# Kernel optimization log

Measured on AMD Instinct MI355X. Metric: run time of the kernel, lower is better.

The kernel has to match this reference:

```python
import jax, jax.numpy as jnp
import numpy as np

VOCAB = 64
D_MODEL = 1024
D_STATE = 128
D_CONV = 4
EXPAND = 2
HEADDIM = 64
N_LAYERS = 4
BATCH, SEQLEN = 4, 4096
D_INNER = EXPAND * D_MODEL            # 2048
NHEADS = D_INNER // HEADDIM           # 32
CONV_DIM = D_INNER + 2 * D_STATE      # 2304 (ngroups=1)
D_IN_PROJ = 2 * D_INNER + 2 * D_STATE + NHEADS  # 4384
EPS = 1e-5


def rmsnorm(x, w):
    return x * jax.lax.rsqrt(jnp.mean(x * x, axis=-1, keepdims=True) + EPS) * w


def setup_inputs() -> dict:
    key = jax.random.key(0)
    ks = jax.random.split(key, 14)
    s = 0.02
    return {
        "x": jax.random.randint(ks[0], (BATCH, SEQLEN), 0, VOCAB),
        "embedding": jax.random.normal(ks[1], (VOCAB, D_MODEL)) * s,
        "in_proj_w": jax.random.normal(ks[2], (N_LAYERS, D_IN_PROJ, D_MODEL)) * s,
        "conv_w": jax.random.normal(ks[3], (N_LAYERS, CONV_DIM, D_CONV)) * s,
        "conv_b": jnp.zeros((N_LAYERS, CONV_DIM)),
        "dt_bias": jax.random.uniform(ks[4], (N_LAYERS, NHEADS), minval=-4.0, maxval=-2.0),
        "A_log": jnp.log(jax.random.uniform(ks[5], (N_LAYERS, NHEADS), minval=1.0, maxval=16.0)),
        "D": jnp.ones((N_LAYERS, NHEADS)),
        "gnorm_w": jnp.ones((N_LAYERS, D_INNER)),
        "out_proj_w": jax.random.normal(ks[6], (N_LAYERS, D_MODEL, D_INNER)) * s,
        "rms_w": jnp.ones((N_LAYERS, D_MODEL)),
        "norm_f_w": jnp.ones((D_MODEL,)),
        "lm_head_w": jax.random.normal(ks[7], (VOCAB, D_MODEL)) * s,
    }


def mamba2_mixer(u, pw, cw, cb, dtb, Alog, Dp, gw, ow):
    b, L, _ = u.shape
    zxbcdt = u @ pw.T                                     # (b,L,D_IN_PROJ)
    z = zxbcdt[..., :D_INNER]
    xBC = zxbcdt[..., D_INNER:D_INNER + CONV_DIM]
    dt = zxbcdt[..., D_INNER + CONV_DIM:]                 # (b,L,H)
    # causal depthwise conv1d + silu
    xpad = jnp.pad(xBC, ((0, 0), (D_CONV - 1, 0), (0, 0)))
    xconv = cb
    for k in range(D_CONV):
        xconv = xconv + xpad[:, k:k + L, :] * cw[:, k]
    xBC = jax.nn.silu(xconv)
    xs = xBC[..., :D_INNER].reshape(b, L, NHEADS, HEADDIM)
    Bm = xBC[..., D_INNER:D_INNER + D_STATE]              # (b,L,N)
    Cm = xBC[..., D_INNER + D_STATE:]                     # (b,L,N)
    dt = jax.nn.softplus(dt + dtb)                        # (b,L,H)
    A = -jnp.exp(Alog)                                    # (H,)
    dA = jnp.exp(dt * A)                                  # (b,L,H)
    dtx = dt[..., None] * xs                              # (b,L,H,P)

    def step(h, inp):
        dA_t, dtx_t, B_t, C_t = inp
        h = dA_t[..., None, None] * h + dtx_t[..., None] * B_t[:, None, None, :]
        y = jnp.einsum('bhpn,bn->bhp', h, C_t)
        return h, y

    h0 = jnp.zeros((b, NHEADS, HEADDIM, D_STATE), u.dtype)
    _, ys = jax.lax.scan(step, h0, (jnp.swapaxes(dA, 0, 1),
                                    jnp.swapaxes(dtx, 0, 1),
                                    jnp.swapaxes(Bm, 0, 1),
                                    jnp.swapaxes(Cm, 0, 1)))
    y = jnp.swapaxes(ys, 0, 1) + Dp[None, None, :, None] * xs
    y = y.reshape(b, L, D_INNER)
    y = rmsnorm(y * jax.nn.silu(z), gw)
    return y @ ow.T


def reference(x, embedding, in_proj_w, conv_w, conv_b, dt_bias, A_log, D,
              gnorm_w, out_proj_w, rms_w, norm_f_w, lm_head_w):
    h = embedding[x]                                      # (b,L,d_model)
    for i in range(N_LAYERS):
        res = h
        h = rmsnorm(h, rms_w[i])
        h = mamba2_mixer(h, in_proj_w[i], conv_w[i], conv_b[i], dt_bias[i],
                         A_log[i], D[i], gnorm_w[i], out_proj_w[i]) + res
    h = rmsnorm(h, norm_f_w)
    return h @ lm_head_w.T                                # (b,L,vocab)
```

## Files before the change

kernel.cpp:

```cpp
#include <hip/hip_runtime.h>
#include <hip/hip_bf16.h>

typedef unsigned short u16;
typedef unsigned int u32;
typedef __attribute__((ext_vector_type(8))) __bf16 bf16x8;
typedef __attribute__((ext_vector_type(4))) float f32x4;

#define SEQ 4096
#define NBATCH 4
#define DMODEL 1024
#define DINNER 2048
#define DSTATE 128
#define NH 32
#define CONVD 2304
#define DPROJ 4384
#define ROWS (NBATCH*SEQ)
#define TCH 256
#define NCH (SEQ/TCH)
#define QS 256
#define NQ (SEQ/QS)
#define XOFF DINNER
#define BOFF (2*DINNER)
#define COFF (2*DINNER + DSTATE)
#define DTOFF (2*DINNER + 2*DSTATE)

__device__ __forceinline__ float bf2f(u16 v) {
    u32 x = ((u32)v) << 16;
    float f;
    __builtin_memcpy(&f, &x, 4);
    return f;
}
__device__ __forceinline__ u16 f2bf(float f) {
    u32 x;
    __builtin_memcpy(&x, &f, 4);
    u32 r = (x + 0x7FFFu + ((x >> 16) & 1u)) >> 16;
    return (u16)r;
}
__device__ __forceinline__ void unpack8(uint4 v, float* f) {
    u32 w0 = v.x, w1 = v.y, w2 = v.z, w3 = v.w;
    f[0] = bf2f((u16)(w0 & 0xFFFF)); f[1] = bf2f((u16)(w0 >> 16));
    f[2] = bf2f((u16)(w1 & 0xFFFF)); f[3] = bf2f((u16)(w1 >> 16));
    f[4] = bf2f((u16)(w2 & 0xFFFF)); f[5] = bf2f((u16)(w2 >> 16));
    f[6] = bf2f((u16)(w3 & 0xFFFF)); f[7] = bf2f((u16)(w3 >> 16));
}

__device__ __forceinline__ void async16(u16* lds_base, const u16* g) {
    __builtin_amdgcn_global_load_lds(
        (const __attribute__((address_space(1))) u32*)g,
        (__attribute__((address_space(3))) u32*)(u32)(size_t)lds_base,
        16, 0, 0);
}

__global__ __launch_bounds__(256) void cvt_kernel(
    const float* __restrict__ in, u16* __restrict__ out, int n)
{
    int i = (blockIdx.x * 256 + threadIdx.x) * 4;
    if (i < n) {
        float4 v = *(const float4*)(in + i);
        u16 o[4] = { f2bf(v.x), f2bf(v.y), f2bf(v.z), f2bf(v.w) };
        *(uint2*)(out + i) = *(const uint2*)o;
    }
}

__global__ __launch_bounds__(256) void embed_kernel(
    const int* __restrict__ x, const float* __restrict__ emb, u16* __restrict__ h)
{
    int row = blockIdx.x, tid = threadIdx.x;
    int id = x[row];
    float4 v = *(const float4*)(emb + (size_t)id * DMODEL + tid * 4);
    u16 o[4] = { f2bf(v.x), f2bf(v.y), f2bf(v.z), f2bf(v.w) };
    *(uint2*)(h + (size_t)row * DMODEL + tid * 4) = *(const uint2*)o;
}

__global__ __launch_bounds__(256) void rmsnorm_kernel(
    const u16* __restrict__ in, const float* __restrict__ w, u16* __restrict__ out)
{
    int row = blockIdx.x, tid = threadIdx.x;
    const u16* r = in + (size_t)row * DMODEL + tid * 4;
    float v[4];
    v[0] = bf2f(r[0]); v[1] = bf2f(r[1]); v[2] = bf2f(r[2]); v[3] = bf2f(r[3]);
    float s = v[0]*v[0] + v[1]*v[1] + v[2]*v[2] + v[3]*v[3];
    #pragma unroll
    for (int off = 32; off; off >>= 1) s += __shfl_xor(s, off);
    __shared__ float red[4];
    if ((tid & 63) == 0) red[tid >> 6] = s;
    __syncthreads();
    float tot = red[0] + red[1] + red[2] + red[3];
    float sc = rsqrtf(tot * (1.f / DMODEL) + 1e-5f);
    float4 wv = *(const float4*)(w + tid * 4);
    u16* o = out + (size_t)row * DMODEL + tid * 4;
    u16 ov[4] = { f2bf(v[0] * sc * wv.x), f2bf(v[1] * sc * wv.y),
                  f2bf(v[2] * sc * wv.z), f2bf(v[3] * sc * wv.w) };
    *(uint2*)o = *(const uint2*)ov;
}

template<int EPI>
__global__ __launch_bounds__(256) void gemm_nt(
    const u16* __restrict__ A, const u16* __restrict__ B,
    int N, int K, int lda, int ntiles,
    u16* __restrict__ Cb, float* __restrict__ Cf)
{
    __shared__ __align__(16) u16 As[128 * 64];
    __shared__ __align__(16) u16 Bs[128 * 64];
    const int GM = 8;
    int gsz = GM * ntiles;
    int bid = blockIdx.x;
    int grp = bid / gsz, rem = bid % gsz;
    int m0 = (grp * GM + (rem % GM)) * 128;
    int n0 = (rem / GM) * 128;

    int tid = threadIdx.x;
    int lane = tid & 63, wv = tid >> 6;
    int wm = wv & 1, wn = wv >> 1;
    int q = lane >> 4, mr = lane & 15;

    f32x4 acc[4][4];
    #pragma unroll
    for (int i = 0; i < 4; i++)
        #pragma unroll
        for (int j = 0; j < 4; j++) acc[i][j] = (f32x4){0.f, 0.f, 0.f, 0.f};

    for (int kt = 0; kt < K; kt += 64) {
        #pragma unroll
        for (int ps = 0; ps < 4; ++ps) {
            int rb = ps * 32 + wv * 8;
            int r = rb + (lane >> 3);
            int scl = (lane & 7) ^ (r & 7);
            async16(&As[rb * 64], A + (size_t)(m0 + r) * lda + kt + scl * 8);
        }
        #pragma unroll
        for (int ps = 0; ps < 4; ++ps) {
            int rb = ps * 32 + wv * 8;
            int r = rb + (lane >> 3);
            int scl = (lane & 7) ^ (r & 7);
            int gn = n0 + r;
            if (gn < N)
                async16(&Bs[rb * 64], B + (size_t)gn * K + kt + scl * 8);
        }
        __syncthreads();
        #pragma unroll
        for (int kk = 0; kk < 2; ++kk) {
            bf16x8 af[4], bfr[4];
            #pragma unroll
            for (int mi = 0; mi < 4; ++mi) {
                int r = wm * 64 + mi * 16 + mr;
                int c = (kk * 4 + q) ^ (r & 7);
                af[mi] = *(const bf16x8*)&As[r * 64 + c * 8];
            }
            #pragma unroll
            for (int ni = 0; ni < 4; ++ni) {
                int r = wn * 64 + ni * 16 + mr;
                int c = (kk * 4 + q) ^ (r & 7);
                bfr[ni] = *(const bf16x8*)&Bs[r * 64 + c * 8];
            }
            #pragma unroll
            for (int mi = 0; mi < 4; ++mi)
                #pragma unroll
                for (int ni = 0; ni < 4; ++ni)
                    acc[mi][ni] = __builtin_amdgcn_mfma_f32_16x16x32_bf16(
                        af[mi], bfr[ni], acc[mi][ni], 0, 0, 0);
        }
        __syncthreads();
    }

    #pragma unroll
    for (int mi = 0; mi < 4; ++mi) {
        #pragma unroll
        for (int ni = 0; ni < 4; ++ni) {
            int gn = n0 + wn * 64 + ni * 16 + mr;
            if (gn < N) {
                #pragma unroll
                for (int r4 = 0; r4 < 4; ++r4) {
                    int gm = m0 + wm * 64 + mi * 16 + q * 4 + r4;
                    float v = acc[mi][ni][r4];
                    size_t idx = (size_t)gm * N + gn;
                    if (EPI == 0)      Cb[idx] = f2bf(v);
                    else if (EPI == 1) Cb[idx] = f2bf(bf2f(Cb[idx]) + v);
                    else               Cf[idx] = v;
                }
            }
        }
    }
}

__global__ __launch_bounds__(256) void halo_kernel(
    const u16* __restrict__ zx, u16* __restrict__ halo)
{
    int c = blockIdx.x * 256 + threadIdx.x;
    int idx = blockIdx.y;
    int b = blockIdx.z;
    int bi = idx / 3, r = idx % 3;
    int t = (bi + 1) * TCH - 3 + r;
    halo[(((size_t)b * (NCH - 1) + bi) * 3 + r) * CONVD + c] =
        zx[((size_t)b * SEQ + t) * DPROJ + DINNER + c];
}

__global__ __launch_bounds__(256) void convip_kernel(
    u16* __restrict__ zx, const float* __restrict__ cw, const float* __restrict__ cb,
    const u16* __restrict__ halo)
{
    int c = blockIdx.x * 256 + threadIdx.x;
    int ci = blockIdx.y;
    int b = blockIdx.z;
    float w0 = cw[c * 4 + 0], w1 = cw[c * 4 + 1];
    float w2 = cw[c * 4 + 2], w3 = cw[c * 4 + 3];
    float bias = cb[c];
    float h3 = 0.f, h2 = 0.f, h1 = 0.f;
    if (ci > 0) {
        const u16* hb = halo + (((size_t)b * (NCH - 1) + (ci - 1)) * 3) * CONVD + c;
        h3 = bf2f(hb[0 * CONVD]);
        h2 = bf2f(hb[1 * CONVD]);
        h1 = bf2f(hb[2 * CONVD]);
    }
    u16* p = zx + ((size_t)b * SEQ + (size_t)ci * TCH) * DPROJ + DINNER + c;
    #pragma unroll 4
    for (int t = 0; t < TCH; ++t) {
        float xr = bf2f(*p);
        float v = bias + w0 * h3 + w1 * h2 + w2 * h1 + w3 * xr;
        *p = f2bf(v / (1.f + expf(-v)));
        h3 = h2; h2 = h1; h1 = xr;
        p += DPROJ;
    }
}

__global__ __launch_bounds__(256) void ssd_p1(
    const u16* __restrict__ zx,
    const float* __restrict__ dtb, const float* __restrict__ Alog,
    u16* __restrict__ cs, float* __restrict__ scum_g, float* __restrict__ sdt_g,
    float* __restrict__ dAck)
{
    int ck = blockIdx.x, hd = blockIdx.y, b = blockIdx.z;
    int tid = threadIdx.x;
    int wv = tid >> 6, lane = tid & 63, q = lane >> 4, mr = lane & 15;

    __shared__ __align__(16) u16 BwT[128 * 136];
    __shared__ __align__(16) u16 XT1[64 * 136];
    __shared__ float scumL[256], sdtL[256], swL[256];

    float An = -expf(Alog[hd]);
    float dtbF = dtb[hd];

    {
        size_t row = (size_t)b * SEQ + ck * QS + tid;
        float xx = bf2f(zx[row * DPROJ + DTOFF + hd]) + dtbF;
        float dt = (xx > 20.f) ? xx : log1pf(expf(xx));
        sdtL[tid] = dt;
        scumL[tid] = dt;
        __syncthreads();
        for (int ofs = 1; ofs < 256; ofs <<= 1) {
            float v = scumL[tid];
            float u = (tid >= ofs) ? scumL[tid - ofs] : 0.f;
            __syncthreads();
            scumL[tid] = v + u;
            __syncthreads();
        }
        float cumQ = scumL[255];
        swL[tid] = expf(An * (cumQ - scumL[tid])) * dt;
        size_t gbase = (((size_t)b * NH + hd) * NQ + ck) * QS;
        scum_g[gbase + tid] = scumL[tid];
        sdt_g[gbase + tid] = dt;
        if (tid == 0) dAck[((size_t)b * NH + hd) * NQ + ck] = expf(An * cumQ);
    }

    f32x4 hacc[2][4];
    #pragma unroll
    for (int i = 0; i < 2; i++)
        #pragma unroll
        for (int j = 0; j < 4; j++) hacc[i][j] = (f32x4){0.f, 0.f, 0.f, 0.f};

    int n0 = wv * 32;
    int jj = tid & 127, hi = tid >> 7;

    for (int half = 0; half < 2; ++half) {
        __syncthreads();
        size_t rowj = ((size_t)b * SEQ + ck * QS + half * 128 + jj) * DPROJ;
        float wj = swL[half * 128 + jj];
        #pragma unroll
        for (int it = 0; it < 8; ++it) {
            int nc = hi * 8 + it;
            uint4 v = *(const uint4*)(zx + rowj + BOFF + nc * 8);
            float f[8]; unpack8(v, f);
            #pragma unroll
            for (int u = 0; u < 8; ++u)
                BwT[(nc * 8 + u) * 136 + jj] = f2bf(f[u] * wj);
        }
        #pragma unroll
        for (int it = 0; it < 4; ++it) {
            int pc = hi * 4 + it;
            uint4 v = *(const uint4*)(zx + rowj + XOFF + hd * 64 + pc * 8);
            const u16* vp = (const u16*)&v;
            #pragma unroll
            for (int u = 0; u < 8; ++u)
                XT1[(pc * 8 + u) * 136 + jj] = vp[u];
        }
        __syncthreads();
        #pragma unroll
        for (int kk = 0; kk < 4; ++kk) {
            bf16x8 af[2], bx[4];
            #pragma unroll
            for (int it = 0; it < 2; ++it)
                af[it] = *(const bf16x8*)&BwT[(n0 + it * 16 + mr) * 136 + kk * 32 + q * 8];
            #pragma unroll
            for (int pt = 0; pt < 4; ++pt)
                bx[pt] = *(const bf16x8*)&XT1[(pt * 16 + mr) * 136 + kk * 32 + q * 8];
            #pragma unroll
            for (int it = 0; it < 2; ++it)
                #pragma unroll
                for (int pt = 0; pt < 4; ++pt)
                    hacc[it][pt] = __builtin_amdgcn_mfma_f32_16x16x32_bf16(
                        af[it], bx[pt], hacc[it][pt], 0, 0, 0);
        }
    }

    size_t basec = (((size_t)b * NH + hd) * NQ + ck) * 8192;
    #pragma unroll
    for (int it = 0; it < 2; ++it)
        #pragma unroll
        for (int pt = 0; pt < 4; ++pt)
            #pragma unroll
            for (int reg = 0; reg < 4; ++reg) {
                int n = n0 + it * 16 + q * 4 + reg;
                int p = pt * 16 + mr;
                cs[basec + p * 128 + n] = f2bf(hacc[it][pt][reg]);
            }
}

__global__ __launch_bounds__(256) void ssd_p2(
    u16* __restrict__ cs, const float* __restrict__ dAck)
{
    int hd = blockIdx.y, b = blockIdx.z;
    int off = blockIdx.x * 1024 + threadIdx.x * 4;
    size_t base = (((size_t)b * NH + hd) * NQ) * 8192 + off;
    const float* dA = dAck + ((size_t)b * NH + hd) * NQ;
    float c0 = 0.f, c1 = 0.f, c2 = 0.f, c3 = 0.f;
    for (int ck = 0; ck < NQ; ++ck) {
        u16* p = cs + base + (size_t)ck * 8192;
        uint2 v = *(const uint2*)p;
        float i0 = bf2f((u16)(v.x & 0xFFFF)), i1 = bf2f((u16)(v.x >> 16));
        float i2 = bf2f((u16)(v.y & 0xFFFF)), i3 = bf2f((u16)(v.y >> 16));
        u16 o[4] = { f2bf(c0), f2bf(c1), f2bf(c2), f2bf(c3) };
        *(uint2*)p = *(const uint2*)o;
        float a = dA[ck];
        c0 = fmaf(a, c0, i0); c1 = fmaf(a, c1, i1);
        c2 = fmaf(a, c2, i2); c3 = fmaf(a, c3, i3);
    }
}

__global__ __launch_bounds__(256, 3) void ssd_p3(
    u16* __restrict__ zx,
    const float* __restrict__ Alog, const float* __restrict__ Dp,
    const u16* __restrict__ cs,
    const float* __restrict__ scum_g, const float* __restrict__ sdt_g)
{
    int ck = blockIdx.x, hd = blockIdx.y, b = blockIdx.z;
    int tid = threadIdx.x;
    int wv = tid >> 6, lane = tid & 63, q = lane >> 4, mr = lane & 15;
    int i0 = wv * 64;

    __shared__ __align__(16) u16 XT[64 * 264];
    __shared__ float scumL[256], sdtL[256];

    float An = -expf(Alog[hd]);
    float Dh = Dp[hd];

    {
        size_t gbase = (((size_t)b * NH + hd) * NQ + ck) * QS;
        scumL[tid] = scum_g[gbase + tid];
        sdtL[tid] = sdt_g[gbase + tid];
    }
    {
        size_t rowj = ((size_t)b * SEQ + ck * QS + tid) * DPROJ + XOFF + hd * 64;
        #pragma unroll
        for (int pc = 0; pc < 8; ++pc) {
            uint4 v = *(const uint4*)(zx + rowj + pc * 8);
            const u16* vp = (const u16*)&v;
            #pragma unroll
            for (int u = 0; u < 8; ++u)
                XT[(pc * 8 + u) * 264 + tid] = vp[u];
        }
    }

    f32x4 Y[4][4];
    #pragma unroll
    for (int i = 0; i < 4; i++)
        #pragma unroll
        for (int j = 0; j < 4; j++) Y[i][j] = (f32x4){0.f, 0.f, 0.f, 0.f};

    const size_t rowC = ((size_t)b * SEQ + ck * QS) * DPROJ;
    size_t basec = (((size_t)b * NH + hd) * NQ + ck) * 8192;

    __syncthreads();

    #pragma unroll
    for (int kk = 0; kk < 4; ++kk) {
        bf16x8 cf[4], hb[4];
        #pragma unroll
        for (int it = 0; it < 4; ++it)
            cf[it] = *(const bf16x8*)(zx + rowC + (size_t)(i0 + it * 16 + mr) * DPROJ
                                      + COFF + kk * 32 + q * 8);
        #pragma unroll
        for (int pt = 0; pt < 4; ++pt)
            hb[pt] = *(const bf16x8*)(cs + basec + (size_t)(pt * 16 + mr) * 128
                                      + kk * 32 + q * 8);
        #pragma unroll
        for (int it = 0; it < 4; ++it)
            #pragma unroll
            for (int pt = 0; pt < 4; ++pt)
                Y[it][pt] = __builtin_amdgcn_mfma_f32_16x16x32_bf16(
                    cf[it], hb[pt], Y[it][pt], 0, 0, 0);
    }
    #pragma unroll
    for (int it = 0; it < 4; ++it)
        #pragma unroll
        for (int reg = 0; reg < 4; ++reg) {
            float f = expf(An * scumL[i0 + it * 16 + q * 4 + reg]);
            #pragma unroll
            for (int pt = 0; pt < 4; ++pt) Y[it][pt][reg] *= f;
        }

    int jtmax = 2 * wv + 2;
    for (int jt = 0; jt < jtmax; ++jt) {
        int jt0 = jt * 32;
        float ref = scumL[jt0 + 15];

        f32x4 ST[2][4];
        #pragma unroll
        for (int jm = 0; jm < 2; ++jm)
            #pragma unroll
            for (int it = 0; it < 4; ++it) ST[jm][it] = (f32x4){0.f, 0.f, 0.f, 0.f};
        #pragma unroll
        for (int kk = 0; kk < 4; ++kk) {
            bf16x8 ba[2], cf[4];
            #pragma unroll
            for (int jm = 0; jm < 2; ++jm)
                ba[jm] = *(const bf16x8*)(zx + rowC + (size_t)(jt0 + jm * 16 + mr) * DPROJ
                                          + BOFF + kk * 32 + q * 8);
            #pragma unroll
            for (int it = 0; it < 4; ++it)
                cf[it] = *(const bf16x8*)(zx + rowC + (size_t)(i0 + it * 16 + mr) * DPROJ
                                          + COFF + kk * 32 + q * 8);
            #pragma unroll
            for (int jm = 0; jm < 2; ++jm)
                #pragma unroll
                for (int it = 0; it < 4; ++it)
                    ST[jm][it] = __builtin_amdgcn_mfma_f32_16x16x32_bf16(
                        ba[jm], cf[it], ST[jm][it], 0, 0, 0);
        }

        int jq = jt0 + (lane & 31);
        float Qv = expf(An * (ref - scumL[jq])) * sdtL[jq];
        float Rit[4];
        #pragma unroll
        for (int it = 0; it < 4; ++it)
            Rit[it] = expf(An * (scumL[i0 + it * 16 + mr] - ref));

        bf16x8 xf[4];
        #pragma unroll
        for (int pt = 0; pt < 4; ++pt)
            xf[pt] = *(const bf16x8*)&XT[(pt * 16 + mr) * 264 + jt0 + q * 8];

        #pragma unroll
        for (int it = 0; it < 4; ++it) {
            u16 marr[8];
            #pragma unroll
            for (int u = 0; u < 8; ++u) {
                int src = (2 * (q & 1) + (u >> 2)) * 16 + mr;
                float s0 = __shfl(ST[0][it][u & 3], src);
                float s1 = __shfl(ST[1][it][u & 3], src);
                float sj = (q < 2) ? s0 : s1;
                float Qu = __shfl(Qv, 8 * q + u);
                int jg = jt0 + 8 * q + u;
                int ig = i0 + it * 16 + mr;
                float m = (jg <= ig) ? Rit[it] * Qu * sj : 0.f;
                marr[u] = f2bf(m);
            }
            bf16x8 mf;
            __builtin_memcpy(&mf, marr, 16);
            #pragma unroll
            for (int pt = 0; pt < 4; ++pt)
                Y[it][pt] = __builtin_amdgcn_mfma_f32_16x16x32_bf16(
                    mf, xf[pt], Y[it][pt], 0, 0, 0);
        }
    }

    #pragma unroll
    for (int it = 0; it < 4; ++it)
        #pragma unroll
        for (int pt = 0; pt < 4; ++pt)
            #pragma unroll
            for (int reg = 0; reg < 4; ++reg) {
                int i = i0 + it * 16 + q * 4 + reg;
                int p = pt * 16 + mr;
                float xv = bf2f(XT[p * 264 + i]);
                float val = Y[it][pt][reg] + Dh * xv;
                zx[((size_t)b * SEQ + ck * QS + i) * DPROJ + XOFF + hd * 64 + p] = f2bf(val);
            }
}

__global__ __launch_bounds__(256) void gatenorm_kernel(
    u16* __restrict__ zx, const float* __restrict__ gw)
{
    int row = blockIdx.x, tid = threadIdx.x;
    u16* zr = zx + (size_t)row * DPROJ;
    float v[8];
    float s = 0.f;
    #pragma unroll
    for (int i = 0; i < 8; ++i) {
        int idx = i * 256 + tid;
        float zv = bf2f(zr[idx]);
        float gate = zv / (1.f + expf(-zv));
        float val = bf2f(zr[DINNER + idx]) * gate;
        v[i] = val;
        s += val * val;
    }
    #pragma unroll
    for (int off = 32; off; off >>= 1) s += __shfl_xor(s, off);
    __shared__ float red[4];
    if ((tid & 63) == 0) red[tid >> 6] = s;
    __syncthreads();
    float tot = red[0] + red[1] + red[2] + red[3];
    float sc = rsqrtf(tot * (1.f / DINNER) + 1e-5f);
    #pragma unroll
    for (int i = 0; i < 8; ++i) {
        int idx = i * 256 + tid;
        zr[DINNER + idx] = f2bf(v[i] * sc * gw[idx]);
    }
}

extern "C" void kernel_launch(void* const* d_in, const int* in_sizes, int n_in,
                              void* d_out, int out_size, void* d_ws, size_t ws_size,
                              hipStream_t stream) {
    const int*   x          = (const int*)d_in[0];
    const float* emb        = (const float*)d_in[1];
    const float* in_proj_w  = (const float*)d_in[2];
    const float* conv_w     = (const float*)d_in[3];
    const float* conv_b     = (const float*)d_in[4];
    const float* dt_bias    = (const float*)d_in[5];
    const float* A_log      = (const float*)d_in[6];
    const float* Dp         = (const float*)d_in[7];
    const float* gnorm_w    = (const float*)d_in[8];
    const float* out_proj_w = (const float*)d_in[9];
    const float* rms_w      = (const float*)d_in[10];
    const float* norm_f_w   = (const float*)d_in[11];
    const float* lm_head_w  = (const float*)d_in[12];
    float* out = (float*)d_out;

    char* w = (char*)d_ws;
    u16* h       = (u16*)w; w += (size_t)ROWS * DMODEL * 2;
    u16* zx      = (u16*)w; w += (size_t)ROWS * DPROJ * 2;
    char* scratch = w;      w += (size_t)NBATCH * NH * NQ * 8192 * 2;
    u16* wA      = (u16*)w; w += (size_t)DPROJ * DMODEL * 2;
    u16* wB      = (u16*)w; w += (size_t)DMODEL * DINNER * 2;
    float* scum_g = (float*)w; w += (size_t)NBATCH * NH * NQ * QS * 4;
    float* sdt_g  = (float*)w; w += (size_t)NBATCH * NH * NQ * QS * 4;
    float* dAck   = (float*)w; w += (size_t)NBATCH * NH * NQ * 4;
    u16* normed  = (u16*)scratch;
    u16* halo    = (u16*)scratch;
    u16* cs      = (u16*)scratch;

    embed_kernel<<<ROWS, 256, 0, stream>>>(x, emb, h);

    const int nInW = DPROJ * DMODEL;
    const int nOutW = DMODEL * DINNER;
    const int nHeadW = 64 * DMODEL;

    for (int l = 0; l < 4; ++l) {
        cvt_kernel<<<nInW / 1024, 256, 0, stream>>>(
            in_proj_w + (size_t)l * nInW, wA, nInW);
        cvt_kernel<<<nOutW / 1024, 256, 0, stream>>>(
            out_proj_w + (size_t)l * nOutW, wB, nOutW);
        rmsnorm_kernel<<<ROWS, 256, 0, stream>>>(h, rms_w + l * DMODEL, normed);
        gemm_nt<0><<<128 * 35, 256, 0, stream>>>(
            normed, wA, DPROJ, DMODEL, DMODEL, 35, zx, nullptr);
        halo_kernel<<<dim3(9, (NCH - 1) * 3, NBATCH), 256, 0, stream>>>(zx, halo);
        convip_kernel<<<dim3(9, NCH, NBATCH), 256, 0, stream>>>(
            zx, conv_w + (size_t)l * CONVD * 4, conv_b + (size_t)l * CONVD, halo);
        ssd_p1<<<dim3(NQ, NH, NBATCH), 256, 0, stream>>>(
            zx, dt_bias + l * NH, A_log + l * NH, cs, scum_g, sdt_g, dAck);
        ssd_p2<<<dim3(8, NH, NBATCH), 256, 0, stream>>>(cs, dAck);
        ssd_p3<<<dim3(NQ, NH, NBATCH), 256, 0, stream>>>(
            zx, A_log + l * NH, Dp + l * NH, cs, scum_g, sdt_g);
        gatenorm_kernel<<<ROWS, 256, 0, stream>>>(zx, gnorm_w + (size_t)l * DINNER);
        gemm_nt<1><<<128 * 8, 256, 0, stream>>>(
            zx + DINNER, wB, DMODEL, DINNER, DPROJ, 8, h, nullptr);
    }

    rmsnorm_kernel<<<ROWS, 256, 0, stream>>>(h, norm_f_w, normed);
    cvt_kernel<<<nHeadW / 1024, 256, 0, stream>>>(lm_head_w, wA, nHeadW);
    gemm_nt<2><<<128 * 1, 256, 0, stream>>>(
        normed, wA, 64, DMODEL, DMODEL, 1, nullptr, out);
}
```

Baseline: 2.724 ms.

## Rework ssd_p3 intra-chunk loop: interleaved row tiles, 16-wide causal tiles, XCD-aware block mapping

The intra-chunk SSD kernel now gives each wave interleaved 16-row tiles instead of a contiguous 64-row band, which balances the causal triangle across waves. It steps over 16-column tiles, skips tiles above the diagonal and masks only on the diagonal tile. This removes the cross-lane shuffles used to rearrange the score tile, and the second matmul switches to the 16x16x16 bf16 MFMA. Blocks are launched on a 1D grid with a remapping that keeps the same (batch, chunk) groups on one XCD for cache locality. Occupancy is raised to 4 blocks per SIMD, at some risk of register spills, and the per-tile work grows because there are more, smaller MFMAs.

```diff
diff --git a/kernel.cpp b/kernel.cpp
--- a/kernel.cpp
+++ b/kernel.cpp
@@ -4,6 +4,8 @@
 typedef unsigned short u16;
 typedef unsigned int u32;
 typedef __attribute__((ext_vector_type(8))) __bf16 bf16x8;
+typedef __attribute__((ext_vector_type(4))) __bf16 bf16x4;
+typedef __attribute__((ext_vector_type(4))) short s16x4;
 typedef __attribute__((ext_vector_type(4))) float f32x4;
 
 #define SEQ 4096
@@ -44,6 +46,20 @@
     f[6] = bf2f((u16)(w3 & 0xFFFF)); f[7] = bf2f((u16)(w3 >> 16));
 }
 
+__device__ __forceinline__ f32x4 mfma16bf(bf16x4 a, bf16x4 b, f32x4 c) {
+#if __has_builtin(__builtin_amdgcn_mfma_f32_16x16x16bf16_1k)
+    s16x4 as, bs;
+    __builtin_memcpy(&as, &a, 8);
+    __builtin_memcpy(&bs, &b, 8);
+    return __builtin_amdgcn_mfma_f32_16x16x16bf16_1k(as, bs, c, 0, 0, 0);
+#else
+    f32x4 d = c;
+    asm volatile("v_mfma_f32_16x16x16_bf16 %0, %1, %2, %0"
+                 : "+v"(d) : "v"(a), "v"(b));
+    return d;
+#endif
+}
+
 __device__ __forceinline__ void async16(u16* lds_base, const u16* g) {
     __builtin_amdgcn_global_load_lds(
         (const __attribute__((address_space(1))) u32*)g,
@@ -346,19 +362,26 @@
     }
 }
 
-__global__ __launch_bounds__(256, 3) void ssd_p3(
+__global__ __launch_bounds__(256, 4) void ssd_p3(
     u16* __restrict__ zx,
     const float* __restrict__ Alog, const float* __restrict__ Dp,
     const u16* __restrict__ cs,
     const float* __restrict__ scum_g, const float* __restrict__ sdt_g)
 {
-    int ck = blockIdx.x, hd = blockIdx.y, b = blockIdx.z;
+    int bid = blockIdx.x;
+    int xcd = bid & 7;
+    int ixd = bid >> 3;
+    int hd  = ixd & 31;
+    int pr  = (xcd << 3) | (ixd >> 5);
+    int b   = pr >> 4;
+    int ck  = pr & 15;
+
     int tid = threadIdx.x;
     int wv = tid >> 6, lane = tid & 63, q = lane >> 4, mr = lane & 15;
-    int i0 = wv * 64;
 
     __shared__ __align__(16) u16 XT[64 * 264];
-    __shared__ float scumL[256], sdtL[256];
+    __shared__ __align__(16) float scumL[256];
+    __shared__ __align__(16) float sdtL[256];
 
     float An = -expf(Alog[hd]);
     float Dh = Dp[hd];
@@ -396,7 +419,7 @@
         bf16x8 cf[4], hb[4];
         #pragma unroll
         for (int it = 0; it < 4; ++it)
-            cf[it] = *(const bf16x8*)(zx + rowC + (size_t)(i0 + it * 16 + mr) * DPROJ
+            cf[it] = *(const bf16x8*)(zx + rowC + (size_t)((wv + 4 * it) * 16 + mr) * DPROJ
                                       + COFF + kk * 32 + q * 8);
         #pragma unroll
         for (int pt = 0; pt < 4; ++pt)
@@ -413,83 +436,78 @@
     for (int it = 0; it < 4; ++it)
         #pragma unroll
         for (int reg = 0; reg < 4; ++reg) {
-            float f = expf(An * scumL[i0 + it * 16 + q * 4 + reg]);
+            float f = expf(An * scumL[(wv + 4 * it) * 16 + q * 4 + reg]);
             #pragma unroll
             for (int pt = 0; pt < 4; ++pt) Y[it][pt][reg] *= f;
         }
 
-    int jtmax = 2 * wv + 2;
-    for (int jt = 0; jt < jtmax; ++jt) {
-        int jt0 = jt * 32;
-        float ref = scumL[jt0 + 15];
-
-        f32x4 ST[2][4];
-        #pragma unroll
-        for (int jm = 0; jm < 2; ++jm)
-            #pragma unroll
-            for (int it = 0; it < 4; ++it) ST[jm][it] = (f32x4){0.f, 0.f, 0.f, 0.f};
+    float sci[4];
+    #pragma unroll
+    for (int it = 0; it < 4; ++it) sci[it] = scumL[(wv + 4 * it) * 16 + mr];
+
+    for (int jt = 0; jt <= wv + 12; ++jt) {
+        f32x4 st[4];
+        #pragma unroll
+        for (int it = 0; it < 4; ++it) st[it] = (f32x4){0.f, 0.f, 0.f, 0.f};
         #pragma unroll
         for (int kk = 0; kk < 4; ++kk) {
-            bf16x8 ba[2], cf[4];
-            #pragma unroll
-            for (int jm = 0; jm < 2; ++jm)
-                ba[jm] = *(const bf16x8*)(zx + rowC + (size_t)(jt0 + jm * 16 + mr) * DPROJ
-                                          + BOFF + kk * 32 + q * 8);
-            #pragma unroll
-            for (int it = 0; it < 4; ++it)
-                cf[it] = *(const bf16x8*)(zx + rowC + (size_t)(i0 + it * 16 + mr) * DPROJ
-                                          + COFF + kk * 32 + q * 8);
-            #pragma unroll
-            for (int jm = 0; jm < 2; ++jm)
+            bf16x8 ba = *(const bf16x8*)(zx + rowC + (size_t)(jt * 16 + mr) * DPROJ
+                                         + BOFF + kk * 32 + q * 8);
+            #pragma unroll
+            for (int it = 0; it < 4; ++it) {
+                if (wv + 4 * it >= jt) {
+                    bf16x8 cf = *(const bf16x8*)(zx + rowC
+                                  + (size_t)((wv + 4 * it) * 16 + mr) * DPROJ
+                                  + COFF + kk * 32 + q * 8);
+                    st[it] = __builtin_amdgcn_mfma_f32_16x16x32_bf16(
+                        ba, cf, st[it], 0, 0, 0);
+                }
+            }
+        }
+
+        float ref = scumL[jt * 16 + 15];
+        float4 scq = *(const float4*)&scumL[jt * 16 + q * 4];
+        float4 sdq = *(const float4*)&sdtL[jt * 16 + q * 4];
+        float Qf[4];
+        Qf[0] = expf(An * (ref - scq.x)) * sdq.x;
+        Qf[1] = expf(An * (ref - scq.y)) * sdq.y;
+        Qf[2] = expf(An * (ref - scq.z)) * sdq.z;
+        Qf[3] = expf(An * (ref - scq.w)) * sdq.w;
+
+        bf16x4 xf[4];
+        #pragma unroll
+        for (int pt = 0; pt < 4; ++pt)
+            xf[pt] = *(const bf16x4*)&XT[(pt * 16 + mr) * 264 + jt * 16 + q * 4];
+
+        #pragma unroll
+        for (int it = 0; it < 4; ++it) {
+            int r = wv + 4 * it;
+            if (r >= jt) {
+                float Ri = expf(An * (sci[it] - ref));
+                bool diag = (r == jt);
+                u16 marr[4];
                 #pragma unroll
-                for (int it = 0; it < 4; ++it)
-                    ST[jm][it] = __builtin_amdgcn_mfma_f32_16x16x32_bf16(
-                        ba[jm], cf[it], ST[jm][it], 0, 0, 0);
-        }
-
-        int jq = jt0 + (lane & 31);
-        float Qv = expf(An * (ref - scumL[jq])) * sdtL[jq];
-        float Rit[4];
-        #pragma unroll
-        for (int it = 0; it < 4; ++it)
-            Rit[it] = expf(An * (scumL[i0 + it * 16 + mr] - ref));
-
-        bf16x8 xf[4];
+                for (int u = 0; u < 4; ++u) {
+                    float m = Ri * Qf[u] * st[it][u];
+                    if (diag && (q * 4 + u > mr)) m = 0.f;
+                    marr[u] = f2bf(m);
+                }
+                bf16x4 mf;
+                __builtin_memcpy(&mf, marr, 8);
+                #pragma unroll
+                for (int pt = 0; pt < 4; ++pt)
+                    Y[it][pt] = mfma16bf(mf, xf[pt], Y[it][pt]);
+            }
+        }
+    }
+
+    #pragma unroll
+    for (int it = 0; it < 4; ++it)
         #pragma unroll
         for (int pt = 0; pt < 4; ++pt)
-            xf[pt] = *(const bf16x8*)&XT[(pt * 16 + mr) * 264 + jt0 + q * 8];
-
-        #pragma unroll
-        for (int it = 0; it < 4; ++it) {
-            u16 marr[8];
-            #pragma unroll
-            for (int u = 0; u < 8; ++u) {
-                int src = (2 * (q & 1) + (u >> 2)) * 16 + mr;
-                float s0 = __shfl(ST[0][it][u & 3], src);
-                float s1 = __shfl(ST[1][it][u & 3], src);
-                float sj = (q < 2) ? s0 : s1;
-                float Qu = __shfl(Qv, 8 * q + u);
-                int jg = jt0 + 8 * q + u;
-                int ig = i0 + it * 16 + mr;
-                float m = (jg <= ig) ? Rit[it] * Qu * sj : 0.f;
-                marr[u] = f2bf(m);
-            }
-            bf16x8 mf;
-            __builtin_memcpy(&mf, marr, 16);
-            #pragma unroll
-            for (int pt = 0; pt < 4; ++pt)
-                Y[it][pt] = __builtin_amdgcn_mfma_f32_16x16x32_bf16(
-                    mf, xf[pt], Y[it][pt], 0, 0, 0);
-        }
-    }
-
-    #pragma unroll
-    for (int it = 0; it < 4; ++it)
-        #pragma unroll
-        for (int pt = 0; pt < 4; ++pt)
             #pragma unroll
             for (int reg = 0; reg < 4; ++reg) {
-                int i = i0 + it * 16 + q * 4 + reg;
+                int i = (wv + 4 * it) * 16 + q * 4 + reg;
                 int p = pt * 16 + mr;
                 float xv = bf2f(XT[p * 264 + i]);
                 float val = Y[it][pt][reg] + Dh * xv;
@@ -578,7 +596,7 @@
         ssd_p1<<<dim3(NQ, NH, NBATCH), 256, 0, stream>>>(
             zx, dt_bias + l * NH, A_log + l * NH, cs, scum_g, sdt_g, dAck);
         ssd_p2<<<dim3(8, NH, NBATCH), 256, 0, stream>>>(cs, dAck);
-        ssd_p3<<<dim3(NQ, NH, NBATCH), 256, 0, stream>>>(
+        ssd_p3<<<NQ * NH * NBATCH, 256, 0, stream>>>(
             zx, A_log + l * NH, Dp + l * NH, cs, scum_g, sdt_g);
         gatenorm_kernel<<<ROWS, 256, 0, stream>>>(zx, gnorm_w + (size_t)l * DINNER);
         gemm_nt<1><<<128 * 8, 256, 0, stream>>>(
```

Result: slower. 2.778 ms (+2.0%).
